# Optimization experiments

Measured on AMD Instinct MI355X. Metric: run time of the kernel, lower is better.

## Reference

```python
import jax, jax.numpy as jnp
import numpy as np


def _mha(x, pos, wq, bq, wk, bk, wv, bv, num_heads):
    # x: (B, S, Din); pos: (S, Din); w*: (Din, Dout); b*: (Dout,)
    x = x + pos  # learned positional embedding, broadcast over batch
    q = x @ wq + bq
    k = x @ wk + bk
    v = x @ wv + bv
    B, S, O = q.shape
    hd = O // num_heads
    q = q.reshape(B, S, num_heads, hd)
    k = k.reshape(B, S, num_heads, hd)
    v = v.reshape(B, S, num_heads, hd)
    scores = jnp.einsum('bshd,bthd->bhst', q, k) / jnp.sqrt(jnp.asarray(hd, x.dtype))
    attn = jax.nn.softmax(scores, axis=-1)
    out = jnp.einsum('bhst,bthd->bshd', attn, v)
    return out.reshape(B, S, O)


def setup_inputs() -> dict:
    key = jax.random.key(0)
    ks = jax.random.split(key, 16)
    B = 16384
    s = 0.3
    f32 = jnp.float32
    return {
        'state': jax.random.normal(ks[0], (B, 100), f32),
        # intraframe attention: Din=1, Dout=2, seq=10, heads=2
        'pos_intra': jax.random.normal(ks[1], (10, 1), f32) * s,
        'wq_intra': jax.random.normal(ks[2], (1, 2), f32) * s,
        'bq_intra': jnp.zeros((2,), f32),
        'wk_intra': jax.random.normal(ks[3], (1, 2), f32) * s,
        'bk_intra': jnp.zeros((2,), f32),
        'wv_intra': jax.random.normal(ks[4], (1, 2), f32) * s,
        'bv_intra': jnp.zeros((2,), f32),
        # interframe attention: Din=20, Dout=21, seq=10, heads=1
        'pos_inter': jax.random.normal(ks[5], (10, 20), f32) * s,
        'wq_inter': jax.random.normal(ks[6], (20, 21), f32) * s,
        'bq_inter': jnp.zeros((21,), f32),
        'wk_inter': jax.random.normal(ks[7], (20, 21), f32) * s,
        'bk_inter': jnp.zeros((21,), f32),
        'wv_inter': jax.random.normal(ks[8], (20, 21), f32) * s,
        'bv_inter': jnp.zeros((21,), f32),
    }


def reference(state, pos_intra, wq_intra, bq_intra, wk_intra, bk_intra,
              wv_intra, bv_intra, pos_inter, wq_inter, bq_inter, wk_inter,
              bk_inter, wv_inter, bv_inter):
    B = state.shape[0]
    # per-sample reshape (10,10,1) fused across the batch: (B*10 frames, 10 tokens, 1 feat)
    frames = state.reshape(B * 10, 10, 1)
    intra = _mha(frames, pos_intra, wq_intra, bq_intra, wk_intra, bk_intra,
                 wv_intra, bv_intra, num_heads=2)          # (B*10, 10, 2)
    x = intra.reshape(B, 10, 20)                            # (B, frames=10, 20)
    out = _mha(x, pos_inter, wq_inter, bq_inter, wk_inter, bk_inter,
               wv_inter, bv_inter, num_heads=1)             # (B, 10, 21)
    return out
```

## Files before the change

kernel.cpp:

```cpp
#include <hip/hip_runtime.h>

typedef __fp16 h2 __attribute__((ext_vector_type(2)));
typedef __fp16 h4 __attribute__((ext_vector_type(4)));
typedef __fp16 h8 __attribute__((ext_vector_type(8)));
typedef float  f4 __attribute__((ext_vector_type(4)));
typedef float  f2 __attribute__((ext_vector_type(2)));

#if __has_builtin(__builtin_amdgcn_fdot2)
#define FDOT2(a, b, c) __builtin_amdgcn_fdot2((a), (b), (c), false)
#else
#define FDOT2(a, b, c) ((c) + (float)(a)[0] * (float)(b)[0] + (float)(a)[1] * (float)(b)[1])
#endif

#define SPB 16
#define NT  320

__device__ __forceinline__ float dpp_xor1(float x) {
    int i = __builtin_amdgcn_mov_dpp(__float_as_int(x), 0xB1, 0xF, 0xF, true);
    return __int_as_float(i);
}

struct SMa {
    __fp16 X [160 * 32];
    __fp16 WT[96 * 32];
};
union UHead { SMa a; float sout[SPB * 210]; };

__global__ __launch_bounds__(NT, 5)
void crazy_attn_kernel(const float* __restrict__ state,
                       const float* __restrict__ pos_intra,
                       const float* __restrict__ wq_i, const float* __restrict__ bq_i,
                       const float* __restrict__ wk_i, const float* __restrict__ bk_i,
                       const float* __restrict__ wv_i, const float* __restrict__ bv_i,
                       const float* __restrict__ pos_inter,
                       const float* __restrict__ wq, const float* __restrict__ bq,
                       const float* __restrict__ wk, const float* __restrict__ bk,
                       const float* __restrict__ wv, const float* __restrict__ bv,
                       float* __restrict__ out, int B)
{
    __shared__ UHead uh;
    __shared__ __fp16 QKV[160 * 72];

    const int tid  = threadIdx.x;
    const int e    = tid & 1;
    const int rr   = (tid >> 1) % 10;
    const int samp = tid / 20;
    const int gs   = blockIdx.x * SPB + samp;
    const int gsc  = (gs < B) ? gs : (B - 1);

    if (tid < 96) {
        const int sec = tid >> 5, within = tid & 31;
        const bool valid = within < 21;
        const float* W  = (sec == 1) ? wk : (sec == 2) ? wv : wq;
        const float* Bb = (sec == 1) ? bk : (sec == 2) ? bv : bq;
        union { uint4 u4[4]; h2 hh[16]; } T;
        #pragma unroll
        for (int p = 0; p < 16; ++p) {
            const int j0 = 2 * p, j1 = 2 * p + 1;
            float lo = 0.f, hi = 0.f;
            if (valid) {
                lo = (j0 < 20) ? W[j0 * 21 + within] : ((j0 == 20) ? Bb[within] : 0.f);
                hi = (j1 < 20) ? W[j1 * 21 + within] : 0.f;
            }
            T.hh[p] = __builtin_amdgcn_cvt_pkrtz(lo, hi);
        }
        uint4* wd = (uint4*)&uh.a.WT[tid * 32];
        wd[0] = T.u4[0]; wd[1] = T.u4[1]; wd[2] = T.u4[2]; wd[3] = T.u4[3];
    }
    __syncthreads();

    {
        const float* sp = state + (size_t)gsc * 100 + rr * 10;
        float xv[10];
        #pragma unroll
        for (int t2 = 0; t2 < 5; ++t2) {
            const f2 v = *(const f2*)&sp[t2 * 2];
            xv[2 * t2]     = v[0] + pos_intra[2 * t2];
            xv[2 * t2 + 1] = v[1] + pos_intra[2 * t2 + 1];
        }
        float xmx = xv[0], xmn = xv[0];
        #pragma unroll
        for (int t = 1; t < 10; ++t) { xmx = fmaxf(xmx, xv[t]); xmn = fminf(xmn, xv[t]); }

        float res[2][5];
        #pragma unroll
        for (int h = 0; h < 2; ++h) {
            const float wqh = wq_i[h], bqh = bq_i[h];
            const float wkh = wk_i[h];
            const float wvh = wv_i[h], bvh = bv_i[h];
            float vh[10];
            #pragma unroll
            for (int t = 0; t < 10; ++t) vh[t] = fmaf(xv[t], wvh, bvh);
            #pragma unroll
            for (int si = 0; si < 5; ++si) {
                const float c0 = fmaf(xv[2 * si],     wqh, bqh) * wkh;
                const float c1 = fmaf(xv[2 * si + 1], wqh, bqh) * wkh;
                const float c  = e ? c1 : c0;
                const float mx = c * ((c >= 0.f) ? xmx : xmn);
                const float cL = c * 1.44269504f;
                const float mL = mx * 1.44269504f;
                float sum = 0.f, o = 0.f;
                #pragma unroll
                for (int t = 0; t < 10; ++t) {
                    const float ex = __builtin_amdgcn_exp2f(fmaf(cL, xv[t], -mL));
                    sum += ex; o = fmaf(ex, vh[t], o);
                }
                res[h][si] = o * __builtin_amdgcn_rcpf(sum);
            }
        }
        __fp16* xrow = &uh.a.X[(samp * 10 + rr) * 32];
        const float* prow = pos_inter + rr * 20;
        #pragma unroll
        for (int si = 0; si < 5; ++si) {
            const int s = 2 * si + e;
            *(h2*)&xrow[2 * s] = __builtin_amdgcn_cvt_pkrtz(res[0][si] + prow[2 * s],
                                                            res[1][si] + prow[2 * s + 1]);
        }
        const h2 z  = __builtin_amdgcn_cvt_pkrtz(0.f, 0.f);
        const h2 bz = __builtin_amdgcn_cvt_pkrtz(1.0f, 0.f);
        #pragma unroll
        for (int j = 0; j < 3; ++j) {
            const int k = 20 + 2 * (3 * e + j);
            *(h2*)&xrow[k] = (e == 0 && j == 0) ? bz : z;
        }
    }

    {
        const int l  = tid & 63;
        const int w  = tid >> 6;
        const int lr = l & 15, lh = l >> 4;
        h8 afrag[6];
        #pragma unroll
        for (int mt = 0; mt < 6; ++mt)
            afrag[mt] = *(const h8*)&uh.a.WT[(mt * 16 + lr) * 32 + lh * 8];
        #pragma unroll
        for (int i = 0; i < 2; ++i) {
            const int xrow = (2 * w + i) * 16 + lr;
            const h8 bfrag = *(const h8*)&uh.a.X[xrow * 32 + lh * 8];
            #pragma unroll
            for (int mt = 0; mt < 6; ++mt) {
                f4 acc = {0.f, 0.f, 0.f, 0.f};
                acc = __builtin_amdgcn_mfma_f32_16x16x32_f16(afrag[mt], bfrag, acc, 0, 0, 0);
                const int m0     = mt * 16 + lh * 4;
                const int sec    = m0 >> 5;
                const int within = m0 & 31;
                if (within <= 20) {
                    union { h2 p2[2]; h4 p4; } P;
                    P.p2[0] = __builtin_amdgcn_cvt_pkrtz(acc[0], acc[1]);
                    P.p2[1] = __builtin_amdgcn_cvt_pkrtz(acc[2], acc[3]);
                    *(h4*)&QKV[xrow * 72 + sec * 24 + within] = P.p4;
                }
            }
        }
    }
    __syncthreads();

    {
        const __fp16* samprows = &QKV[samp * 10 * 72];
        union { uint4 u4[3]; h2 hh[12]; } Q;
        {
            const uint4* qsrc = (const uint4*)&samprows[rr * 72];
            Q.u4[0] = qsrc[0]; Q.u4[1] = qsrc[1]; Q.u4[2] = qsrc[2];
        }
        float mysc[5];
        #pragma unroll
        for (int i = 0; i < 5; ++i) {
            const int t = 2 * i + e;
            union { uint4 u4[3]; h2 hh[12]; } K;
            const uint4* ks = (const uint4*)&samprows[t * 72 + 24];
            K.u4[0] = ks[0]; K.u4[1] = ks[1]; K.u4[2] = ks[2];
            float d = 0.f;
            #pragma unroll
            for (int p = 0; p < 11; ++p) d = FDOT2(Q.hh[p], K.hh[p], d);
            mysc[i] = d * 0.21821789023599239f;
        }
        float mymax = mysc[0];
        #pragma unroll
        for (int i = 1; i < 5; ++i) mymax = fmaxf(mymax, mysc[i]);
        const float m = fmaxf(mymax, dpp_xor1(mymax));
        float pe[5], psum = 0.f;
        #pragma unroll
        for (int i = 0; i < 5; ++i) {
            pe[i] = __builtin_amdgcn_exp2f((mysc[i] - m) * 1.44269504f);
            psum += pe[i];
        }
        const float sum = psum + dpp_xor1(psum);
        const float inv = __builtin_amdgcn_rcpf(sum);

        float acc[21];
        #pragma unroll
        for (int c = 0; c < 21; ++c) acc[c] = 0.f;
        #pragma unroll
        for (int i = 0; i < 5; ++i) {
            const int t = 2 * i + e;
            union { uint4 u4[3]; h2 hh[12]; } V;
            const uint4* vs = (const uint4*)&samprows[t * 72 + 48];
            V.u4[0] = vs[0]; V.u4[1] = vs[1]; V.u4[2] = vs[2];
            const float a = pe[i] * inv;
            #pragma unroll
            for (int c = 0; c < 21; ++c)
                acc[c] = fmaf(a, (float)V.hh[c >> 1][c & 1], acc[c]);
        }
        #pragma unroll
        for (int c = 0; c < 21; ++c) acc[c] += dpp_xor1(acc[c]);
        if (e == 0) {
            float* dst = &uh.sout[(samp * 10 + rr) * 21];
            #pragma unroll
            for (int c = 0; c < 21; ++c) dst[c] = acc[c];
        }
    }
    __syncthreads();

    {
        const int samp0 = blockIdx.x * SPB;
        const int nrem  = B - samp0;
        const int nval  = ((nrem < SPB) ? nrem : SPB) * 210;
        float* gdst = out + (size_t)samp0 * 210;
        if (nval == SPB * 210) {
            for (int i = tid; i < SPB * 210 / 4; i += NT)
                ((f4*)gdst)[i] = ((const f4*)uh.sout)[i];
        } else {
            for (int i = tid; i < nval; i += NT) gdst[i] = uh.sout[i];
        }
    }
}

extern "C" void kernel_launch(void* const* d_in, const int* in_sizes, int n_in,
                              void* d_out, int out_size, void* d_ws, size_t ws_size,
                              hipStream_t stream) {
    const float* state     = (const float*)d_in[0];
    const float* pos_intra = (const float*)d_in[1];
    const float* wq_i      = (const float*)d_in[2];
    const float* bq_i      = (const float*)d_in[3];
    const float* wk_i      = (const float*)d_in[4];
    const float* bk_i      = (const float*)d_in[5];
    const float* wv_i      = (const float*)d_in[6];
    const float* bv_i      = (const float*)d_in[7];
    const float* pos_inter = (const float*)d_in[8];
    const float* wq        = (const float*)d_in[9];
    const float* bq        = (const float*)d_in[10];
    const float* wk        = (const float*)d_in[11];
    const float* bk        = (const float*)d_in[12];
    const float* wv        = (const float*)d_in[13];
    const float* bv        = (const float*)d_in[14];
    float* outp = (float*)d_out;

    const int B = in_sizes[0] / 100;
    const int grid = (B + SPB - 1) / SPB;
    hipLaunchKernelGGL(crazy_attn_kernel, dim3(grid), dim3(NT), 0, stream,
                       state, pos_intra, wq_i, bq_i, wk_i, bk_i, wv_i, bv_i,
                       pos_inter, wq, bq, wk, bk, wv, bv, outp, B);
}
```

Baseline: 22.19 us.

## Double threads per block, split intra-frame heads across lanes, fold V projection

```diff
diff --git a/kernel.cpp b/kernel.cpp
--- a/kernel.cpp
+++ b/kernel.cpp
@@ -13,7 +13,7 @@
 #endif
 
 #define SPB 16
-#define NT  320
+#define NT  640
 
 __device__ __forceinline__ float dpp_xor1(float x) {
     int i = __builtin_amdgcn_mov_dpp(__float_as_int(x), 0xB1, 0xF, 0xF, true);
@@ -26,7 +26,7 @@
 };
 union UHead { SMa a; float sout[SPB * 210]; };
 
-__global__ __launch_bounds__(NT, 5)
+__global__ __launch_bounds__(NT, 8)
 void crazy_attn_kernel(const float* __restrict__ state,
                        const float* __restrict__ pos_intra,
                        const float* __restrict__ wq_i, const float* __restrict__ bq_i,
@@ -42,9 +42,10 @@
     __shared__ __fp16 QKV[160 * 72];
 
     const int tid  = threadIdx.x;
-    const int e    = tid & 1;
-    const int rr   = (tid >> 1) % 10;
-    const int samp = tid / 20;
+    const int samp = tid / 40;
+    const int u    = tid - samp * 40;
+    const int r    = u >> 2;
+    const int e4   = u & 3;
     const int gs   = blockIdx.x * SPB + samp;
     const int gsc  = (gs < B) ? gs : (B - 1);
 
@@ -70,7 +71,7 @@
     __syncthreads();
 
     {
-        const float* sp = state + (size_t)gsc * 100 + rr * 10;
+        const float* sp = state + (size_t)gsc * 100 + r * 10;
         float xv[10];
         #pragma unroll
         for (int t2 = 0; t2 < 5; ++t2) {
@@ -82,46 +83,38 @@
         #pragma unroll
         for (int t = 1; t < 10; ++t) { xmx = fmaxf(xmx, xv[t]); xmn = fminf(xmn, xv[t]); }
 
-        float res[2][5];
-        #pragma unroll
-        for (int h = 0; h < 2; ++h) {
-            const float wqh = wq_i[h], bqh = bq_i[h];
-            const float wkh = wk_i[h];
-            const float wvh = wv_i[h], bvh = bv_i[h];
-            float vh[10];
-            #pragma unroll
-            for (int t = 0; t < 10; ++t) vh[t] = fmaf(xv[t], wvh, bvh);
-            #pragma unroll
-            for (int si = 0; si < 5; ++si) {
-                const float c0 = fmaf(xv[2 * si],     wqh, bqh) * wkh;
-                const float c1 = fmaf(xv[2 * si + 1], wqh, bqh) * wkh;
-                const float c  = e ? c1 : c0;
-                const float mx = c * ((c >= 0.f) ? xmx : xmn);
-                const float cL = c * 1.44269504f;
-                const float mL = mx * 1.44269504f;
-                float sum = 0.f, o = 0.f;
-                #pragma unroll
-                for (int t = 0; t < 10; ++t) {
-                    const float ex = __builtin_amdgcn_exp2f(fmaf(cL, xv[t], -mL));
-                    sum += ex; o = fmaf(ex, vh[t], o);
-                }
-                res[h][si] = o * __builtin_amdgcn_rcpf(sum);
+        const int h  = e4 >> 1;
+        const int sh = e4 & 1;
+        const float wqh = h ? wq_i[1] : wq_i[0];
+        const float bqh = h ? bq_i[1] : bq_i[0];
+        const float wkh = h ? wk_i[1] : wk_i[0];
+        const float wvh = h ? wv_i[1] : wv_i[0];
+        const float bvh = h ? bv_i[1] : bv_i[0];
+
+        __fp16* xrow = &uh.a.X[(samp * 10 + r) * 32];
+        const float* prow = pos_inter + r * 20;
+        #pragma unroll
+        for (int si = 0; si < 5; ++si) {
+            const float c0 = fmaf(xv[2 * si],     wqh, bqh) * wkh;
+            const float c1 = fmaf(xv[2 * si + 1], wqh, bqh) * wkh;
+            const float c  = sh ? c1 : c0;
+            const float mx = c * ((c >= 0.f) ? xmx : xmn);
+            const float cL = c * 1.44269504f;
+            const float mL = mx * 1.44269504f;
+            float S0 = 0.f, S1 = 0.f;
+            #pragma unroll
+            for (int t = 0; t < 10; ++t) {
+                const float ex = __builtin_amdgcn_exp2f(fmaf(cL, xv[t], -mL));
+                S0 += ex; S1 = fmaf(ex, xv[t], S1);
             }
-        }
-        __fp16* xrow = &uh.a.X[(samp * 10 + rr) * 32];
-        const float* prow = pos_inter + rr * 20;
-        #pragma unroll
-        for (int si = 0; si < 5; ++si) {
-            const int s = 2 * si + e;
-            *(h2*)&xrow[2 * s] = __builtin_amdgcn_cvt_pkrtz(res[0][si] + prow[2 * s],
-                                                            res[1][si] + prow[2 * s + 1]);
-        }
-        const h2 z  = __builtin_amdgcn_cvt_pkrtz(0.f, 0.f);
-        const h2 bz = __builtin_amdgcn_cvt_pkrtz(1.0f, 0.f);
+            const float res = fmaf(wvh, S1 * __builtin_amdgcn_rcpf(S0), bvh);
+            const int k = 4 * si + 2 * sh + h;
+            xrow[k] = (__fp16)(res + prow[k]);
+        }
         #pragma unroll
         for (int j = 0; j < 3; ++j) {
-            const int k = 20 + 2 * (3 * e + j);
-            *(h2*)&xrow[k] = (e == 0 && j == 0) ? bz : z;
+            const int k = 20 + 4 * j + e4;
+            xrow[k] = (__fp16)((k == 20) ? 1.0f : 0.0f);
         }
     }
 
@@ -133,33 +126,31 @@
         #pragma unroll
         for (int mt = 0; mt < 6; ++mt)
             afrag[mt] = *(const h8*)&uh.a.WT[(mt * 16 + lr) * 32 + lh * 8];
-        #pragma unroll
-        for (int i = 0; i < 2; ++i) {
-            const int xrow = (2 * w + i) * 16 + lr;
-            const h8 bfrag = *(const h8*)&uh.a.X[xrow * 32 + lh * 8];
-            #pragma unroll
-            for (int mt = 0; mt < 6; ++mt) {
-                f4 acc = {0.f, 0.f, 0.f, 0.f};
-                acc = __builtin_amdgcn_mfma_f32_16x16x32_f16(afrag[mt], bfrag, acc, 0, 0, 0);
-                const int m0     = mt * 16 + lh * 4;
-                const int sec    = m0 >> 5;
-                const int within = m0 & 31;
-                if (within <= 20) {
-                    union { h2 p2[2]; h4 p4; } P;
-                    P.p2[0] = __builtin_amdgcn_cvt_pkrtz(acc[0], acc[1]);
-                    P.p2[1] = __builtin_amdgcn_cvt_pkrtz(acc[2], acc[3]);
-                    *(h4*)&QKV[xrow * 72 + sec * 24 + within] = P.p4;
-                }
+        const int xrow = w * 16 + lr;
+        const h8 bfrag = *(const h8*)&uh.a.X[xrow * 32 + lh * 8];
+        #pragma unroll
+        for (int mt = 0; mt < 6; ++mt) {
+            f4 acc = {0.f, 0.f, 0.f, 0.f};
+            acc = __builtin_amdgcn_mfma_f32_16x16x32_f16(afrag[mt], bfrag, acc, 0, 0, 0);
+            const int m0     = mt * 16 + lh * 4;
+            const int sec    = m0 >> 5;
+            const int within = m0 & 31;
+            if (within <= 20) {
+                union { h2 p2[2]; h4 p4; } P;
+                P.p2[0] = __builtin_amdgcn_cvt_pkrtz(acc[0], acc[1]);
+                P.p2[1] = __builtin_amdgcn_cvt_pkrtz(acc[2], acc[3]);
+                *(h4*)&QKV[xrow * 72 + sec * 24 + within] = P.p4;
             }
         }
     }
     __syncthreads();
 
-    {
-        const __fp16* samprows = &QKV[samp * 10 * 72];
+    if (e4 < 2) {
+        const int e = e4;
+        const __fp16* samprows = &QKV[samp * 720];
         union { uint4 u4[3]; h2 hh[12]; } Q;
         {
-            const uint4* qsrc = (const uint4*)&samprows[rr * 72];
+            const uint4* qsrc = (const uint4*)&samprows[r * 72];
             Q.u4[0] = qsrc[0]; Q.u4[1] = qsrc[1]; Q.u4[2] = qsrc[2];
         }
         float mysc[5];
@@ -204,7 +195,7 @@
         #pragma unroll
         for (int c = 0; c < 21; ++c) acc[c] += dpp_xor1(acc[c]);
         if (e == 0) {
-            float* dst = &uh.sout[(samp * 10 + rr) * 21];
+            float* dst = &uh.sout[(samp * 10 + r) * 21];
             #pragma unroll
             for (int c = 0; c < 21; ++c) dst[c] = acc[c];
         }
```

Measured after the change: 29.46 us. 1.33x slower.
